# Performance work log

Measured on AMD Instinct MI355X. Metric: run time of the kernel, lower is better.

## Reference

```python
import jax, jax.numpy as jnp
import numpy as np

EPSILON = 1e-13
LN_EPS = 1e-5
DIRECTIONS = 2
HID = 512


def setup_inputs() -> dict:
    key = jax.random.key(0)
    k1, k2, k3, k4 = jax.random.split(key, 4)
    B, N, D = 16, 1024, HID
    adj = jax.random.randint(k1, (B, N, N), 0, 3, dtype=jnp.int32)  # labels 0..2
    hid = jax.random.normal(k2, (B, N, D), dtype=jnp.float32)
    W = jax.random.normal(k3, (DIRECTIONS * D, D), dtype=jnp.float32) * (1.0 / np.sqrt(DIRECTIONS * D))
    b = jnp.zeros((D,), dtype=jnp.float32)
    gamma = jnp.ones((D,), dtype=jnp.float32)
    beta = jnp.zeros((D,), dtype=jnp.float32)
    return {"adj": adj, "hid": hid, "W": W, "b": b, "gamma": gamma, "beta": beta}


def _layer_norm(x, gamma, beta):
    mu = jnp.mean(x, axis=-1, keepdims=True)
    var = jnp.mean(jnp.square(x - mu), axis=-1, keepdims=True)
    return (x - mu) * jax.lax.rsqrt(var + LN_EPS) * gamma + beta


def reference(adj, hid, W, b, gamma, beta):
    residual = hid
    direct_list = []
    for j in range(DIRECTIONS):  # fixed small structural loop
        mask = (adj == (j + 1)).astype(hid.dtype)            # [B,N,N]
        weight = mask / (jnp.sum(mask, axis=-1, keepdims=True) + EPSILON)
        direct_list.append(jnp.einsum('bnm,bmd->bnd', weight, hid))
    out = jnp.concatenate(direct_list, axis=-1)              # [B,N,directions*D]
    out = out @ W + b                                        # [B,N,D]
    out = jax.nn.relu(out)
    out = out + residual
    return _layer_norm(out, gamma, beta)
```

## Files before the change

kernel.cpp:

```cpp
#include <hip/hip_runtime.h>

#define NB 16
#define NN 1024
#define ND 512

typedef __attribute__((ext_vector_type(8))) short short8;
typedef __attribute__((ext_vector_type(4))) float f32x4;

typedef const __attribute__((address_space(1))) void* gptr1;
typedef __attribute__((address_space(3))) void* lptr3;

static __device__ __forceinline__ unsigned f2bf(float f) {
  union { float f; unsigned u; } v; v.f = f;
  unsigned r = v.u + 0x7FFFu + ((v.u >> 16) & 1u);
  return r >> 16;
}

__global__ void k_count(const int* __restrict__ adj, float* __restrict__ invc) {
  int row = blockIdx.x * 4 + (threadIdx.x >> 6);
  int lane = threadIdx.x & 63;
  const int4* p = (const int4*)(adj + (size_t)row * NN);
  int c1 = 0, c2 = 0;
#pragma unroll
  for (int i = 0; i < 4; ++i) {
    int4 v = p[lane + 64 * i];
    c1 += (v.x == 1) + (v.y == 1) + (v.z == 1) + (v.w == 1);
    c2 += (v.x == 2) + (v.y == 2) + (v.z == 2) + (v.w == 2);
  }
#pragma unroll
  for (int o = 32; o; o >>= 1) { c1 += __shfl_xor(c1, o); c2 += __shfl_xor(c2, o); }
  if (lane == 0) {
    invc[row * 2 + 0] = 1.0f / ((float)c1 + 1e-13f);
    invc[row * 2 + 1] = 1.0f / ((float)c2 + 1e-13f);
  }
}

__global__ void k_transpose_cvt(const float* __restrict__ hid, const float* __restrict__ W,
                                unsigned short* __restrict__ hidT, unsigned short* __restrict__ WT) {
  __shared__ float t[64][65];
  int z = blockIdx.z;
  const float* src; unsigned short* dst;
  if (z < NB) { src = hid + (size_t)z * NN * ND; dst = hidT + (size_t)z * ND * NN; }
  else        { src = W;                          dst = WT; }
  int r0 = blockIdx.x * 64;
  int c0 = blockIdx.y * 64;
  int tid = threadIdx.x;
#pragma unroll
  for (int i = 0; i < 4; ++i) {
    int f = i * 256 + tid;
    int r = f >> 4, cq = f & 15;
    float4 v = *(const float4*)(src + (size_t)(r0 + r) * ND + c0 + cq * 4);
    t[r][cq * 4 + 0] = v.x; t[r][cq * 4 + 1] = v.y;
    t[r][cq * 4 + 2] = v.z; t[r][cq * 4 + 3] = v.w;
  }
  __syncthreads();
#pragma unroll
  for (int i = 0; i < 8; ++i) {
    int f = i * 256 + tid;
    int oc = f >> 5;
    int on = (f & 31) * 2;
    unsigned lo = f2bf(t[on][oc]), hi = f2bf(t[on + 1][oc]);
    *(unsigned*)(dst + (size_t)(c0 + oc) * NN + r0 + on) = lo | (hi << 16);
  }
}

__global__ __launch_bounds__(256, 2) void k_agg(
    const int* __restrict__ adj, const unsigned short* __restrict__ hidT,
    const float* __restrict__ invc, unsigned short* __restrict__ Y) {
  __shared__ __align__(16) char smem[49152];
  char* A1 = smem;
  char* A2 = smem + 16384;
  char* Bt = smem + 32768;

  int phys = blockIdx.x;
  int logical = (phys & 7) * 64 + (phys >> 3);
  int b  = logical >> 5;
  int rem = logical & 31;
  int mt = rem >> 2, nt = rem & 3;
  int m0 = mt * 128, n0 = nt * 128;

  int tid = threadIdx.x;
  int lane = tid & 63, wid = tid >> 6;
  int wr = wid >> 1, wc = wid & 1;

  const int* adjb = adj + (size_t)b * NN * NN;
  const unsigned short* hTb = hidT + (size_t)b * ND * NN;

  f32x4 acc1[4][4], acc2[4][4];
  f32x4 zero = {0.f, 0.f, 0.f, 0.f};
#pragma unroll
  for (int i = 0; i < 4; ++i)
#pragma unroll
    for (int j = 0; j < 4; ++j) { acc1[i][j] = zero; acc2[i][j] = zero; }

  for (int kt = 0; kt < 16; ++kt) {
    int k0 = kt * 64;
    __syncthreads();
#pragma unroll
    for (int it = 0; it < 8; ++it) {
      int f = it * 256 + tid;
      int row = f >> 4, colq = f & 15;
      int4 v = *(const int4*)(adjb + (size_t)(m0 + row) * NN + k0 + colq * 4);
      unsigned m1a = (v.x == 1 ? 0x3F80u : 0u) | (v.y == 1 ? 0x3F800000u : 0u);
      unsigned m1b = (v.z == 1 ? 0x3F80u : 0u) | (v.w == 1 ? 0x3F800000u : 0u);
      unsigned m2a = (v.x == 2 ? 0x3F80u : 0u) | (v.y == 2 ? 0x3F800000u : 0u);
      unsigned m2b = (v.z == 2 ? 0x3F80u : 0u) | (v.w == 2 ? 0x3F800000u : 0u);
      int addr = row * 128 + (((colq >> 1) ^ (row & 7)) * 16) + (colq & 1) * 8;
      *(uint2*)(A1 + addr) = make_uint2(m1a, m1b);
      *(uint2*)(A2 + addr) = make_uint2(m2a, m2b);
    }
#pragma unroll
    for (int i = 0; i < 4; ++i) {
      int q = wid * 4 + i;
      int c = q * 8 + (lane >> 3);
      int s = (lane & 7) ^ (c & 7);
      const unsigned short* src = hTb + (size_t)(n0 + c) * NN + k0 + s * 8;
      __builtin_amdgcn_global_load_lds((gptr1)src, (lptr3)(Bt + q * 1024), 16, 0, 0);
    }
    __syncthreads();
#pragma unroll
    for (int ks = 0; ks < 2; ++ks) {
      short8 a1[4], a2[4], bf[4];
#pragma unroll
      for (int mi = 0; mi < 4; ++mi) {
        int row = wr * 64 + mi * 16 + (lane & 15);
        int slot = (ks * 4 + (lane >> 4)) ^ (row & 7);
        a1[mi] = *(const short8*)(A1 + row * 128 + slot * 16);
        a2[mi] = *(const short8*)(A2 + row * 128 + slot * 16);
      }
#pragma unroll
      for (int nj = 0; nj < 4; ++nj) {
        int col = wc * 64 + nj * 16 + (lane & 15);
        int slot = (ks * 4 + (lane >> 4)) ^ (col & 7);
        bf[nj] = *(const short8*)(Bt + col * 128 + slot * 16);
      }
#pragma unroll
      for (int mi = 0; mi < 4; ++mi)
#pragma unroll
        for (int nj = 0; nj < 4; ++nj) {
          acc1[mi][nj] = __builtin_amdgcn_mfma_f32_16x16x32_bf16(a1[mi], bf[nj], acc1[mi][nj], 0, 0, 0);
          acc2[mi][nj] = __builtin_amdgcn_mfma_f32_16x16x32_bf16(a2[mi], bf[nj], acc2[mi][nj], 0, 0, 0);
        }
    }
  }
  unsigned short* Yb = Y + (size_t)b * NN * (2 * ND);
#pragma unroll
  for (int mi = 0; mi < 4; ++mi) {
#pragma unroll
    for (int rr = 0; rr < 4; ++rr) {
      int grow = m0 + wr * 64 + mi * 16 + (lane >> 4) * 4 + rr;
      float i1 = invc[((size_t)b * NN + grow) * 2 + 0];
      float i2 = invc[((size_t)b * NN + grow) * 2 + 1];
#pragma unroll
      for (int nj = 0; nj < 4; ++nj) {
        int col = n0 + wc * 64 + nj * 16 + (lane & 15);
        Yb[(size_t)grow * 1024 + col]       = (unsigned short)f2bf(acc1[mi][nj][rr] * i1);
        Yb[(size_t)grow * 1024 + 512 + col] = (unsigned short)f2bf(acc2[mi][nj][rr] * i2);
      }
    }
  }
}

__global__ __launch_bounds__(256, 2) void k_out(
    const unsigned short* __restrict__ Y, const unsigned short* __restrict__ WT,
    const float* __restrict__ bias, const float* __restrict__ hid,
    float* __restrict__ out) {
  __shared__ __align__(16) char smem[32768];
  char* At = smem;
  char* Bt = smem + 16384;

  int phys = blockIdx.x;
  int logical = (phys & 7) * 64 + (phys >> 3);
  int mt = logical >> 2, nt = logical & 3;
  int m0 = mt * 128, n0 = nt * 128;

  int tid = threadIdx.x, lane = tid & 63, wid = tid >> 6;
  int wr = wid >> 1, wc = wid & 1;

  f32x4 acc[4][4];
  f32x4 zero = {0.f, 0.f, 0.f, 0.f};
#pragma unroll
  for (int i = 0; i < 4; ++i)
#pragma unroll
    for (int j = 0; j < 4; ++j) acc[i][j] = zero;

  for (int kt = 0; kt < 16; ++kt) {
    int k0 = kt * 64;
    __syncthreads();
#pragma unroll
    for (int i = 0; i < 4; ++i) {
      int q = wid * 4 + i;
      int r = q * 8 + (lane >> 3);
      int s = (lane & 7) ^ (r & 7);
      const unsigned short* src = Y + (size_t)(m0 + r) * 1024 + k0 + s * 8;
      __builtin_amdgcn_global_load_lds((gptr1)src, (lptr3)(At + q * 1024), 16, 0, 0);
    }
#pragma unroll
    for (int i = 0; i < 4; ++i) {
      int q = wid * 4 + i;
      int c = q * 8 + (lane >> 3);
      int s = (lane & 7) ^ (c & 7);
      const unsigned short* src = WT + (size_t)(n0 + c) * 1024 + k0 + s * 8;
      __builtin_amdgcn_global_load_lds((gptr1)src, (lptr3)(Bt + q * 1024), 16, 0, 0);
    }
    __syncthreads();
#pragma unroll
    for (int ks = 0; ks < 2; ++ks) {
      short8 af[4], bf[4];
#pragma unroll
      for (int mi = 0; mi < 4; ++mi) {
        int row = wr * 64 + mi * 16 + (lane & 15);
        int slot = (ks * 4 + (lane >> 4)) ^ (row & 7);
        af[mi] = *(const short8*)(At + row * 128 + slot * 16);
      }
#pragma unroll
      for (int nj = 0; nj < 4; ++nj) {
        int col = wc * 64 + nj * 16 + (lane & 15);
        int slot = (ks * 4 + (lane >> 4)) ^ (col & 7);
        bf[nj] = *(const short8*)(Bt + col * 128 + slot * 16);
      }
#pragma unroll
      for (int mi = 0; mi < 4; ++mi)
#pragma unroll
        for (int nj = 0; nj < 4; ++nj)
          acc[mi][nj] = __builtin_amdgcn_mfma_f32_16x16x32_bf16(af[mi], bf[nj], acc[mi][nj], 0, 0, 0);
    }
  }
#pragma unroll
  for (int mi = 0; mi < 4; ++mi) {
#pragma unroll
    for (int rr = 0; rr < 4; ++rr) {
      int grow = m0 + wr * 64 + mi * 16 + (lane >> 4) * 4 + rr;
#pragma unroll
      for (int nj = 0; nj < 4; ++nj) {
        int col = n0 + wc * 64 + nj * 16 + (lane & 15);
        float v = acc[mi][nj][rr] + bias[col];
        v = fmaxf(v, 0.f);
        v += hid[(size_t)grow * ND + col];
        out[(size_t)grow * ND + col] = v;
      }
    }
  }
}

__global__ void k_ln(float* __restrict__ out, const float* __restrict__ gamma,
                     const float* __restrict__ beta) {
  int row = blockIdx.x * 4 + (threadIdx.x >> 6);
  int lane = threadIdx.x & 63;
  float* p = out + (size_t)row * ND;
  float4 x0 = *(const float4*)(p + lane * 4);
  float4 x1 = *(const float4*)(p + 256 + lane * 4);
  float s = x0.x + x0.y + x0.z + x0.w + x1.x + x1.y + x1.z + x1.w;
#pragma unroll
  for (int o = 32; o; o >>= 1) s += __shfl_xor(s, o);
  float mu = s * (1.0f / 512.0f);
  float d0x = x0.x - mu, d0y = x0.y - mu, d0z = x0.z - mu, d0w = x0.w - mu;
  float d1x = x1.x - mu, d1y = x1.y - mu, d1z = x1.z - mu, d1w = x1.w - mu;
  float v = d0x * d0x + d0y * d0y + d0z * d0z + d0w * d0w
          + d1x * d1x + d1y * d1y + d1z * d1z + d1w * d1w;
#pragma unroll
  for (int o = 32; o; o >>= 1) v += __shfl_xor(v, o);
  float rs = rsqrtf(v * (1.0f / 512.0f) + 1e-5f);
  float4 g0 = *(const float4*)(gamma + lane * 4);
  float4 g1 = *(const float4*)(gamma + 256 + lane * 4);
  float4 b0 = *(const float4*)(beta + lane * 4);
  float4 b1 = *(const float4*)(beta + 256 + lane * 4);
  float4 y0, y1;
  y0.x = d0x * rs * g0.x + b0.x; y0.y = d0y * rs * g0.y + b0.y;
  y0.z = d0z * rs * g0.z + b0.z; y0.w = d0w * rs * g0.w + b0.w;
  y1.x = d1x * rs * g1.x + b1.x; y1.y = d1y * rs * g1.y + b1.y;
  y1.z = d1z * rs * g1.z + b1.z; y1.w = d1w * rs * g1.w + b1.w;
  *(float4*)(p + lane * 4) = y0;
  *(float4*)(p + 256 + lane * 4) = y1;
}

extern "C" void kernel_launch(void* const* d_in, const int* in_sizes, int n_in,
                              void* d_out, int out_size, void* d_ws, size_t ws_size,
                              hipStream_t stream) {
  (void)in_sizes; (void)n_in; (void)out_size; (void)ws_size;
  const int*   adj   = (const int*)d_in[0];
  const float* hid   = (const float*)d_in[1];
  const float* W     = (const float*)d_in[2];
  const float* bias  = (const float*)d_in[3];
  const float* gamma = (const float*)d_in[4];
  const float* beta  = (const float*)d_in[5];
  float* out = (float*)d_out;

  char* ws = (char*)d_ws;
  float*          invc = (float*)ws;
  unsigned short* hidT = (unsigned short*)(ws + 131072);
  unsigned short* WT   = (unsigned short*)(ws + 16908288);
  unsigned short* Y    = (unsigned short*)(ws + 17956864);
  k_count<<<4096, 256, 0, stream>>>(adj, invc);
  k_transpose_cvt<<<dim3(16, 8, 17), 256, 0, stream>>>(hid, W, hidT, WT);
  k_agg<<<512, 256, 0, stream>>>(adj, hidT, invc, Y);
  k_out<<<512, 256, 0, stream>>>(Y, WT, bias, hid, out);
  k_ln<<<4096, 256, 0, stream>>>(out, gamma, beta);
}
```

Baseline: 111.1 us.

## Reassociate to project hid by W first, fuse row counts into aggregation GEMM

```diff
diff --git a/kernel.cpp b/kernel.cpp
--- a/kernel.cpp
+++ b/kernel.cpp
@@ -9,6 +9,10 @@
 
 typedef const __attribute__((address_space(1))) void* gptr1;
 typedef __attribute__((address_space(3))) void* lptr3;
+
+#define VMCNT0() asm volatile("s_waitcnt vmcnt(0)" ::: "memory")
+#define LGKM0()  asm volatile("s_waitcnt lgkmcnt(0)" ::: "memory")
+#define BAR()    __builtin_amdgcn_s_barrier()
 
 static __device__ __forceinline__ unsigned f2bf(float f) {
   union { float f; unsigned u; } v; v.f = f;
@@ -16,32 +20,8 @@
   return r >> 16;
 }
 
-__global__ void k_count(const int* __restrict__ adj, float* __restrict__ invc) {
-  int row = blockIdx.x * 4 + (threadIdx.x >> 6);
-  int lane = threadIdx.x & 63;
-  const int4* p = (const int4*)(adj + (size_t)row * NN);
-  int c1 = 0, c2 = 0;
-#pragma unroll
-  for (int i = 0; i < 4; ++i) {
-    int4 v = p[lane + 64 * i];
-    c1 += (v.x == 1) + (v.y == 1) + (v.z == 1) + (v.w == 1);
-    c2 += (v.x == 2) + (v.y == 2) + (v.z == 2) + (v.w == 2);
-  }
-#pragma unroll
-  for (int o = 32; o; o >>= 1) { c1 += __shfl_xor(c1, o); c2 += __shfl_xor(c2, o); }
-  if (lane == 0) {
-    invc[row * 2 + 0] = 1.0f / ((float)c1 + 1e-13f);
-    invc[row * 2 + 1] = 1.0f / ((float)c2 + 1e-13f);
-  }
-}
-
-__global__ void k_transpose_cvt(const float* __restrict__ hid, const float* __restrict__ W,
-                                unsigned short* __restrict__ hidT, unsigned short* __restrict__ WT) {
+__global__ void k_wt(const float* __restrict__ W, unsigned short* __restrict__ WT) {
   __shared__ float t[64][65];
-  int z = blockIdx.z;
-  const float* src; unsigned short* dst;
-  if (z < NB) { src = hid + (size_t)z * NN * ND; dst = hidT + (size_t)z * ND * NN; }
-  else        { src = W;                          dst = WT; }
   int r0 = blockIdx.x * 64;
   int c0 = blockIdx.y * 64;
   int tid = threadIdx.x;
@@ -49,7 +29,7 @@
   for (int i = 0; i < 4; ++i) {
     int f = i * 256 + tid;
     int r = f >> 4, cq = f & 15;
-    float4 v = *(const float4*)(src + (size_t)(r0 + r) * ND + c0 + cq * 4);
+    float4 v = *(const float4*)(W + (size_t)(r0 + r) * ND + c0 + cq * 4);
     t[r][cq * 4 + 0] = v.x; t[r][cq * 4 + 1] = v.y;
     t[r][cq * 4 + 2] = v.z; t[r][cq * 4 + 3] = v.w;
   }
@@ -60,31 +40,29 @@
     int oc = f >> 5;
     int on = (f & 31) * 2;
     unsigned lo = f2bf(t[on][oc]), hi = f2bf(t[on + 1][oc]);
-    *(unsigned*)(dst + (size_t)(c0 + oc) * NN + r0 + on) = lo | (hi << 16);
-  }
-}
-
-__global__ __launch_bounds__(256, 2) void k_agg(
-    const int* __restrict__ adj, const unsigned short* __restrict__ hidT,
-    const float* __restrict__ invc, unsigned short* __restrict__ Y) {
+    *(unsigned*)(WT + (size_t)(c0 + oc) * NN + r0 + on) = lo | (hi << 16);
+  }
+}
+
+__global__ __launch_bounds__(256, 2) void k_pre(
+    const float* __restrict__ hid, const unsigned short* __restrict__ WT,
+    unsigned short* __restrict__ Pt1, unsigned short* __restrict__ Pt2) {
   __shared__ __align__(16) char smem[49152];
   char* A1 = smem;
   char* A2 = smem + 16384;
-  char* Bt = smem + 32768;
+  char* Bh = smem + 32768;
 
   int phys = blockIdx.x;
   int logical = (phys & 7) * 64 + (phys >> 3);
-  int b  = logical >> 5;
+  int b = logical >> 5;
   int rem = logical & 31;
-  int mt = rem >> 2, nt = rem & 3;
-  int m0 = mt * 128, n0 = nt * 128;
-
-  int tid = threadIdx.x;
-  int lane = tid & 63, wid = tid >> 6;
+  int dt = rem >> 3, mt = rem & 7;
+  int d0 = dt * 128, m0 = mt * 128;
+
+  int tid = threadIdx.x, lane = tid & 63, wid = tid >> 6;
   int wr = wid >> 1, wc = wid & 1;
 
-  const int* adjb = adj + (size_t)b * NN * NN;
-  const unsigned short* hTb = hidT + (size_t)b * ND * NN;
+  const float* hb = hid + (size_t)b * NN * ND;
 
   f32x4 acc1[4][4], acc2[4][4];
   f32x4 zero = {0.f, 0.f, 0.f, 0.f};
@@ -93,14 +71,162 @@
 #pragma unroll
     for (int j = 0; j < 4; ++j) { acc1[i][j] = zero; acc2[i][j] = zero; }
 
-  for (int kt = 0; kt < 16; ++kt) {
+  float4 fc[8], fn[8];
+#pragma unroll
+  for (int it = 0; it < 8; ++it) {
+    int f = it * 256 + tid;
+    fc[it] = *(const float4*)(hb + (size_t)(m0 + (f >> 4)) * ND + (f & 15) * 4);
+  }
+#pragma unroll
+  for (int i = 0; i < 4; ++i) {
+    int q = wid * 4 + i;
+    int r = q * 8 + (lane >> 3);
+    int sl = (lane & 7) ^ (r & 7);
+    __builtin_amdgcn_global_load_lds((gptr1)(WT + (size_t)(d0 + r) * NN + sl * 8),
+                                     (lptr3)(A1 + q * 1024), 16, 0, 0);
+    __builtin_amdgcn_global_load_lds((gptr1)(WT + (size_t)(d0 + r) * NN + 512 + sl * 8),
+                                     (lptr3)(A2 + q * 1024), 16, 0, 0);
+  }
+
+  for (int kt = 0; kt < 8; ++kt) {
     int k0 = kt * 64;
-    __syncthreads();
 #pragma unroll
     for (int it = 0; it < 8; ++it) {
       int f = it * 256 + tid;
       int row = f >> 4, colq = f & 15;
-      int4 v = *(const int4*)(adjb + (size_t)(m0 + row) * NN + k0 + colq * 4);
+      float4 v = fc[it];
+      unsigned lo = f2bf(v.x) | (f2bf(v.y) << 16);
+      unsigned hi = f2bf(v.z) | (f2bf(v.w) << 16);
+      int addr = row * 128 + (((colq >> 1) ^ (row & 7)) * 16) + (colq & 1) * 8;
+      *(uint2*)(Bh + addr) = make_uint2(lo, hi);
+    }
+    VMCNT0();
+    if (kt < 7) {
+#pragma unroll
+      for (int it = 0; it < 8; ++it) {
+        int f = it * 256 + tid;
+        fn[it] = *(const float4*)(hb + (size_t)(m0 + (f >> 4)) * ND + k0 + 64 + (f & 15) * 4);
+      }
+    }
+    LGKM0();
+    BAR();
+#pragma unroll
+    for (int ks = 0; ks < 2; ++ks) {
+      short8 a1[4], a2[4], bf[4];
+#pragma unroll
+      for (int mi = 0; mi < 4; ++mi) {
+        int row = wr * 64 + mi * 16 + (lane & 15);
+        int slot = (ks * 4 + (lane >> 4)) ^ (row & 7);
+        a1[mi] = *(const short8*)(A1 + row * 128 + slot * 16);
+        a2[mi] = *(const short8*)(A2 + row * 128 + slot * 16);
+      }
+#pragma unroll
+      for (int nj = 0; nj < 4; ++nj) {
+        int col = wc * 64 + nj * 16 + (lane & 15);
+        int slot = (ks * 4 + (lane >> 4)) ^ (col & 7);
+        bf[nj] = *(const short8*)(Bh + col * 128 + slot * 16);
+      }
+#pragma unroll
+      for (int mi = 0; mi < 4; ++mi)
+#pragma unroll
+        for (int nj = 0; nj < 4; ++nj) {
+          acc1[mi][nj] = __builtin_amdgcn_mfma_f32_16x16x32_bf16(a1[mi], bf[nj], acc1[mi][nj], 0, 0, 0);
+          acc2[mi][nj] = __builtin_amdgcn_mfma_f32_16x16x32_bf16(a2[mi], bf[nj], acc2[mi][nj], 0, 0, 0);
+        }
+    }
+    BAR();
+    if (kt < 7) {
+#pragma unroll
+      for (int i = 0; i < 4; ++i) {
+        int q = wid * 4 + i;
+        int r = q * 8 + (lane >> 3);
+        int sl = (lane & 7) ^ (r & 7);
+        __builtin_amdgcn_global_load_lds((gptr1)(WT + (size_t)(d0 + r) * NN + k0 + 64 + sl * 8),
+                                         (lptr3)(A1 + q * 1024), 16, 0, 0);
+        __builtin_amdgcn_global_load_lds((gptr1)(WT + (size_t)(d0 + r) * NN + 512 + k0 + 64 + sl * 8),
+                                         (lptr3)(A2 + q * 1024), 16, 0, 0);
+      }
+#pragma unroll
+      for (int it = 0; it < 8; ++it) fc[it] = fn[it];
+    }
+  }
+  unsigned short* P1b = Pt1 + (size_t)b * ND * NN;
+  unsigned short* P2b = Pt2 + (size_t)b * ND * NN;
+#pragma unroll
+  for (int mi = 0; mi < 4; ++mi) {
+#pragma unroll
+    for (int rr = 0; rr < 4; ++rr) {
+      int rowd = d0 + wr * 64 + mi * 16 + (lane >> 4) * 4 + rr;
+#pragma unroll
+      for (int nj = 0; nj < 4; ++nj) {
+        int colm = m0 + wc * 64 + nj * 16 + (lane & 15);
+        P1b[(size_t)rowd * NN + colm] = (unsigned short)f2bf(acc1[mi][nj][rr]);
+        P2b[(size_t)rowd * NN + colm] = (unsigned short)f2bf(acc2[mi][nj][rr]);
+      }
+    }
+  }
+}
+
+__global__ __launch_bounds__(256, 2) void k_main(
+    const int* __restrict__ adj, const unsigned short* __restrict__ Pt1,
+    const unsigned short* __restrict__ Pt2, const float* __restrict__ bias,
+    const float* __restrict__ hid, float* __restrict__ out) {
+  __shared__ __align__(16) char smem[65536];
+  char* A1 = smem;
+  char* A2 = smem + 16384;
+  char* B1 = smem + 32768;
+  char* B2 = smem + 49152;
+
+  int phys = blockIdx.x;
+  int logical = (phys & 7) * 64 + (phys >> 3);
+  int b = logical >> 5;
+  int rem = logical & 31;
+  int mt = rem >> 2, nt = rem & 3;
+  int n0 = mt * 128, d0 = nt * 128;
+
+  int tid = threadIdx.x, lane = tid & 63, wid = tid >> 6;
+  int wr = wid >> 1, wc = wid & 1;
+
+  const int* adjb = adj + (size_t)b * NN * NN;
+  const unsigned short* P1b = Pt1 + (size_t)b * ND * NN;
+  const unsigned short* P2b = Pt2 + (size_t)b * ND * NN;
+
+  f32x4 acc1[4][4], acc2[4][4], cnt1[4], cnt2[4];
+  f32x4 zero = {0.f, 0.f, 0.f, 0.f};
+#pragma unroll
+  for (int i = 0; i < 4; ++i) {
+    cnt1[i] = zero; cnt2[i] = zero;
+#pragma unroll
+    for (int j = 0; j < 4; ++j) { acc1[i][j] = zero; acc2[i][j] = zero; }
+  }
+  short8 ones;
+#pragma unroll
+  for (int i = 0; i < 8; ++i) ones[i] = (short)0x3F80;
+
+  int4 vc[8], vn[8];
+#pragma unroll
+  for (int it = 0; it < 8; ++it) {
+    int f = it * 256 + tid;
+    vc[it] = *(const int4*)(adjb + (size_t)(n0 + (f >> 4)) * NN + (f & 15) * 4);
+  }
+#pragma unroll
+  for (int i = 0; i < 4; ++i) {
+    int q = wid * 4 + i;
+    int r = q * 8 + (lane >> 3);
+    int sl = (lane & 7) ^ (r & 7);
+    __builtin_amdgcn_global_load_lds((gptr1)(P1b + (size_t)(d0 + r) * NN + sl * 8),
+                                     (lptr3)(B1 + q * 1024), 16, 0, 0);
+    __builtin_amdgcn_global_load_lds((gptr1)(P2b + (size_t)(d0 + r) * NN + sl * 8),
+                                     (lptr3)(B2 + q * 1024), 16, 0, 0);
+  }
+
+  for (int kt = 0; kt < 16; ++kt) {
+    int k0 = kt * 64;
+#pragma unroll
+    for (int it = 0; it < 8; ++it) {
+      int f = it * 256 + tid;
+      int row = f >> 4, colq = f & 15;
+      int4 v = vc[it];
       unsigned m1a = (v.x == 1 ? 0x3F80u : 0u) | (v.y == 1 ? 0x3F800000u : 0u);
       unsigned m1b = (v.z == 1 ? 0x3F80u : 0u) | (v.w == 1 ? 0x3F800000u : 0u);
       unsigned m2a = (v.x == 2 ? 0x3F80u : 0u) | (v.y == 2 ? 0x3F800000u : 0u);
@@ -109,18 +235,19 @@
       *(uint2*)(A1 + addr) = make_uint2(m1a, m1b);
       *(uint2*)(A2 + addr) = make_uint2(m2a, m2b);
     }
-#pragma unroll
-    for (int i = 0; i < 4; ++i) {
-      int q = wid * 4 + i;
-      int c = q * 8 + (lane >> 3);
-      int s = (lane & 7) ^ (c & 7);
-      const unsigned short* src = hTb + (size_t)(n0 + c) * NN + k0 + s * 8;
-      __builtin_amdgcn_global_load_lds((gptr1)src, (lptr3)(Bt + q * 1024), 16, 0, 0);
-    }
-    __syncthreads();
+    VMCNT0();
+    if (kt < 15) {
+#pragma unroll
+      for (int it = 0; it < 8; ++it) {
+        int f = it * 256 + tid;
+        vn[it] = *(const int4*)(adjb + (size_t)(n0 + (f >> 4)) * NN + k0 + 64 + (f & 15) * 4);
+      }
+    }
+    LGKM0();
+    BAR();
 #pragma unroll
     for (int ks = 0; ks < 2; ++ks) {
-      short8 a1[4], a2[4], bf[4];
+      short8 a1[4], a2[4], b1[4], b2[4];
 #pragma unroll
       for (int mi = 0; mi < 4; ++mi) {
         int row = wr * 64 + mi * 16 + (lane & 15);
@@ -132,112 +259,51 @@
       for (int nj = 0; nj < 4; ++nj) {
         int col = wc * 64 + nj * 16 + (lane & 15);
         int slot = (ks * 4 + (lane >> 4)) ^ (col & 7);
-        bf[nj] = *(const short8*)(Bt + col * 128 + slot * 16);
-      }
-#pragma unroll
-      for (int mi = 0; mi < 4; ++mi)
+        b1[nj] = *(const short8*)(B1 + col * 128 + slot * 16);
+        b2[nj] = *(const short8*)(B2 + col * 128 + slot * 16);
+      }
+#pragma unroll
+      for (int mi = 0; mi < 4; ++mi) {
+        cnt1[mi] = __builtin_amdgcn_mfma_f32_16x16x32_bf16(a1[mi], ones, cnt1[mi], 0, 0, 0);
+        cnt2[mi] = __builtin_amdgcn_mfma_f32_16x16x32_bf16(a2[mi], ones, cnt2[mi], 0, 0, 0);
 #pragma unroll
         for (int nj = 0; nj < 4; ++nj) {
-          acc1[mi][nj] = __builtin_amdgcn_mfma_f32_16x16x32_bf16(a1[mi], bf[nj], acc1[mi][nj], 0, 0, 0);
-          acc2[mi][nj] = __builtin_amdgcn_mfma_f32_16x16x32_bf16(a2[mi], bf[nj], acc2[mi][nj], 0, 0, 0);
+          acc1[mi][nj] = __builtin_amdgcn_mfma_f32_16x16x32_bf16(a1[mi], b1[nj], acc1[mi][nj], 0, 0, 0);
+          acc2[mi][nj] = __builtin_amdgcn_mfma_f32_16x16x32_bf16(a2[mi], b2[nj], acc2[mi][nj], 0, 0, 0);
         }
-    }
-  }
-  unsigned short* Yb = Y + (size_t)b * NN * (2 * ND);
+      }
+    }
+    BAR();
+    if (kt < 15) {
+#pragma unroll
+      for (int i = 0; i < 4; ++i) {
+        int q = wid * 4 + i;
+        int r = q * 8 + (lane >> 3);
+        int sl = (lane & 7) ^ (r & 7);
+        __builtin_amdgcn_global_load_lds((gptr1)(P1b + (size_t)(d0 + r) * NN + k0 + 64 + sl * 8),
+                                         (lptr3)(B1 + q * 1024), 16, 0, 0);
+        __builtin_amdgcn_global_load_lds((gptr1)(P2b + (size_t)(d0 + r) * NN + k0 + 64 + sl * 8),
+                                         (lptr3)(B2 + q * 1024), 16, 0, 0);
+      }
+#pragma unroll
+      for (int it = 0; it < 8; ++it) vc[it] = vn[it];
+    }
+  }
 #pragma unroll
   for (int mi = 0; mi < 4; ++mi) {
 #pragma unroll
     for (int rr = 0; rr < 4; ++rr) {
-      int grow = m0 + wr * 64 + mi * 16 + (lane >> 4) * 4 + rr;
-      float i1 = invc[((size_t)b * NN + grow) * 2 + 0];
-      float i2 = invc[((size_t)b * NN + grow) * 2 + 1];
+      int n = n0 + wr * 64 + mi * 16 + (lane >> 4) * 4 + rr;
+      float i1 = 1.0f / (cnt1[mi][rr] + 1e-13f);
+      float i2 = 1.0f / (cnt2[mi][rr] + 1e-13f);
+      const float* hrow = hid + ((size_t)b * NN + n) * ND;
+      float* orow = out + ((size_t)b * NN + n) * ND;
 #pragma unroll
       for (int nj = 0; nj < 4; ++nj) {
-        int col = n0 + wc * 64 + nj * 16 + (lane & 15);
-        Yb[(size_t)grow * 1024 + col]       = (unsigned short)f2bf(acc1[mi][nj][rr] * i1);
-        Yb[(size_t)grow * 1024 + 512 + col] = (unsigned short)f2bf(acc2[mi][nj][rr] * i2);
-      }
-    }
-  }
-}
-
-__global__ __launch_bounds__(256, 2) void k_out(
-    const unsigned short* __restrict__ Y, const unsigned short* __restrict__ WT,
-    const float* __restrict__ bias, const float* __restrict__ hid,
-    float* __restrict__ out) {
-  __shared__ __align__(16) char smem[32768];
-  char* At = smem;
-  char* Bt = smem + 16384;
-
-  int phys = blockIdx.x;
-  int logical = (phys & 7) * 64 + (phys >> 3);
-  int mt = logical >> 2, nt = logical & 3;
-  int m0 = mt * 128, n0 = nt * 128;
-
-  int tid = threadIdx.x, lane = tid & 63, wid = tid >> 6;
-  int wr = wid >> 1, wc = wid & 1;
-
-  f32x4 acc[4][4];
-  f32x4 zero = {0.f, 0.f, 0.f, 0.f};
-#pragma unroll
-  for (int i = 0; i < 4; ++i)
-#pragma unroll
-    for (int j = 0; j < 4; ++j) acc[i][j] = zero;
-
-  for (int kt = 0; kt < 16; ++kt) {
-    int k0 = kt * 64;
-    __syncthreads();
-#pragma unroll
-    for (int i = 0; i < 4; ++i) {
-      int q = wid * 4 + i;
-      int r = q * 8 + (lane >> 3);
-      int s = (lane & 7) ^ (r & 7);
-      const unsigned short* src = Y + (size_t)(m0 + r) * 1024 + k0 + s * 8;
-      __builtin_amdgcn_global_load_lds((gptr1)src, (lptr3)(At + q * 1024), 16, 0, 0);
-    }
-#pragma unroll
-    for (int i = 0; i < 4; ++i) {
-      int q = wid * 4 + i;
-      int c = q * 8 + (lane >> 3);
-      int s = (lane & 7) ^ (c & 7);
-      const unsigned short* src = WT + (size_t)(n0 + c) * 1024 + k0 + s * 8;
-      __builtin_amdgcn_global_load_lds((gptr1)src, (lptr3)(Bt + q * 1024), 16, 0, 0);
-    }
-    __syncthreads();
-#pragma unroll
-    for (int ks = 0; ks < 2; ++ks) {
-      short8 af[4], bf[4];
-#pragma unroll
-      for (int mi = 0; mi < 4; ++mi) {
-        int row = wr * 64 + mi * 16 + (lane & 15);
-        int slot = (ks * 4 + (lane >> 4)) ^ (row & 7);
-        af[mi] = *(const short8*)(At + row * 128 + slot * 16);
-      }
-#pragma unroll
-      for (int nj = 0; nj < 4; ++nj) {
-        int col = wc * 64 + nj * 16 + (lane & 15);
-        int slot = (ks * 4 + (lane >> 4)) ^ (col & 7);
-        bf[nj] = *(const short8*)(Bt + col * 128 + slot * 16);
-      }
-#pragma unroll
-      for (int mi = 0; mi < 4; ++mi)
-#pragma unroll
-        for (int nj = 0; nj < 4; ++nj)
-          acc[mi][nj] = __builtin_amdgcn_mfma_f32_16x16x32_bf16(af[mi], bf[nj], acc[mi][nj], 0, 0, 0);
-    }
-  }
-#pragma unroll
-  for (int mi = 0; mi < 4; ++mi) {
-#pragma unroll
-    for (int rr = 0; rr < 4; ++rr) {
-      int grow = m0 + wr * 64 + mi * 16 + (lane >> 4) * 4 + rr;
-#pragma unroll
-      for (int nj = 0; nj < 4; ++nj) {
-        int col = n0 + wc * 64 + nj * 16 + (lane & 15);
-        float v = acc[mi][nj][rr] + bias[col];
+        int d = d0 + wc * 64 + nj * 16 + (lane & 15);
+        float v = acc1[mi][nj][rr] * i1 + acc2[mi][nj][rr] * i2 + bias[d];
         v = fmaxf(v, 0.f);
-        v += hid[(size_t)grow * ND + col];
-        out[(size_t)grow * ND + col] = v;
+        orow[d] = v + hrow[d];
       }
     }
   }
@@ -287,13 +353,12 @@
   float* out = (float*)d_out;
 
   char* ws = (char*)d_ws;
-  float*          invc = (float*)ws;
-  unsigned short* hidT = (unsigned short*)(ws + 131072);
-  unsigned short* WT   = (unsigned short*)(ws + 16908288);
-  unsigned short* Y    = (unsigned short*)(ws + 17956864);
-  k_count<<<4096, 256, 0, stream>>>(adj, invc);
-  k_transpose_cvt<<<dim3(16, 8, 17), 256, 0, stream>>>(hid, W, hidT, WT);
-  k_agg<<<512, 256, 0, stream>>>(adj, hidT, invc, Y);
-  k_out<<<512, 256, 0, stream>>>(Y, WT, bias, hid, out);
-  k_ln<<<4096, 256, 0, stream>>>(out, gamma, beta);
-}
+  unsigned short* WT  = (unsigned short*)ws;
+  unsigned short* Pt1 = (unsigned short*)(ws + 1048576);
+  unsigned short* Pt2 = (unsigned short*)(ws + 17825792);
+
+  k_wt  <<<dim3(16, 8), 256, 0, stream>>>(W, WT);
+  k_pre <<<512, 256, 0, stream>>>(hid, WT, Pt1, Pt2);
+  k_main<<<512, 256, 0, stream>>>(adj, Pt1, Pt2, bias, hid, out);
+  k_ln  <<<4096, 256, 0, stream>>>(out, gamma, beta);
+}
```

Result: slower. 148.0 us (+33.1%).
